# Optimization experiments

Hardware: AMD Instinct MI355X
Metric: run time of the kernel (lower is better)

## Reference

```python
import jax, jax.numpy as jnp
import numpy as np

B, L, D, H = 2, 4096, 128, 4


def setup_inputs() -> dict:
    key = jax.random.key(0)
    k_x, k_q, k_k, k_v, k_o = jax.random.split(key, 5)
    std = 0.02
    x = jax.random.normal(k_x, (B, L, D), dtype=jnp.float32)
    # torch nn.Linear(d_model, H*d_model).weight has shape [H*D, D]
    Wq = std * jax.random.normal(k_q, (H * D, D), dtype=jnp.float32)
    Wk = std * jax.random.normal(k_k, (H * D, D), dtype=jnp.float32)
    Wv = std * jax.random.normal(k_v, (H * D, D), dtype=jnp.float32)
    # W_O: Linear(H*d_model, d_model).weight -> [D, H*D]
    Wo = std * jax.random.normal(k_o, (D, H * D), dtype=jnp.float32)
    return {"x": x, "Wq": Wq, "Wk": Wk, "Wv": Wv, "Wo": Wo}


def reference(x, Wq, Wk, Wv, Wo):
    # project: weight rows indexed by (h, e); out = x @ W^T
    Wq3 = Wq.reshape(H, D, D)
    Wk3 = Wk.reshape(H, D, D)
    Wv3 = Wv.reshape(H, D, D)
    q = jnp.einsum('bld,hed->bhle', x, Wq3)  # [B,H,L,D]
    k = jnp.einsum('bld,hed->bhle', x, Wk3)
    v = jnp.einsum('bld,hed->bhle', x, Wv3)
    logits = jnp.einsum('bhle,bhme->bhlm', q, k)  # [B,H,L,L]
    causal_mask = jnp.triu(jnp.ones((L, L), dtype=bool), 1)
    neg = jnp.finfo(logits.dtype).min
    logits = jnp.where(causal_mask, neg, logits)
    attn = jax.nn.softmax(logits, axis=-1)
    ctx = jnp.einsum('bhlm,bhme->bhle', attn, v)  # [B,H,L,D]
    ctx = ctx.transpose(0, 2, 1, 3).reshape(B, L, H * D)
    y = ctx @ Wo.T  # [B,L,D]
    return y
```

## Files before the change

### kernel.cpp

```cpp
#include <hip/hip_runtime.h>

#define BB 2
#define LL 4096
#define DD 128
#define HH 4

typedef unsigned short u16;
typedef unsigned int u32;
typedef __attribute__((ext_vector_type(8))) short short8;
typedef __attribute__((ext_vector_type(4))) float floatx4;

union PFrag { short8 s; u32 u[4]; };

__device__ __forceinline__ u16 f2bf(float f) {
    union { float f; u32 u; } v; v.f = f;
    return (u16)((v.u + 0x7fffu + ((v.u >> 16) & 1u)) >> 16);
}

__device__ __forceinline__ void gld16(const u16* g, u16* l) {
    __builtin_amdgcn_global_load_lds((const __attribute__((address_space(1))) void*)g,
                                     (__attribute__((address_space(3))) void*)l, 16, 0, 0);
}

__device__ __forceinline__ int pfx(int t) {
    return (t < 16) ? (t - 8) : (t < 24) ? 8 + (t - 16) * 2 : 24 + (t - 24) * 3;
}

__global__ __launch_bounds__(256) void cvt_all(const float* __restrict__ x,
                                               const float* __restrict__ wq,
                                               const float* __restrict__ wk,
                                               const float* __restrict__ wv,
                                               const float* __restrict__ wo,
                                               u16* xb, u16* wqb, u16* wkb,
                                               u16* wvb, u16* wob,
                                               float* l_acc) {
    int z = blockIdx.y;
    if (z == 5) {
        int i = (blockIdx.x * 256 + threadIdx.x) * 4;
        if (i < 8 * LL) *(float4*)(l_acc + i) = (float4){0.f, 0.f, 0.f, 0.f};
        return;
    }
    const float* src; u16* dst; int n;
    if      (z == 0) { src = x;  dst = xb;  n = BB * LL * DD; }
    else if (z == 1) { src = wq; dst = wqb; n = HH * DD * DD; }
    else if (z == 2) { src = wk; dst = wkb; n = HH * DD * DD; }
    else if (z == 3) { src = wv; dst = wvb; n = HH * DD * DD; }
    else             { src = wo; dst = wob; n = DD * HH * DD; }
    int i = (blockIdx.x * 256 + threadIdx.x) * 4;
    if (i >= n) return;
    float4 v = *(const float4*)(src + i);
    ushort4 o;
    o.x = f2bf(v.x); o.y = f2bf(v.y); o.z = f2bf(v.z); o.w = f2bf(v.w);
    *(ushort4*)(dst + i) = o;
}

__global__ __launch_bounds__(256) void proj_qkv(const u16* __restrict__ xb,
                                                const u16* __restrict__ wqb,
                                                const u16* __restrict__ wkb,
                                                const u16* __restrict__ wvb,
                                                u16* __restrict__ Qb,
                                                u16* __restrict__ Kb,
                                                u16* __restrict__ Vt) {
    __shared__ __align__(16) u16 At[128 * 128];
    __shared__ __align__(16) u16 Wt[128 * 128];
    int lane = threadIdx.x & 63;
    int w    = threadIdx.x >> 6;
    int c = lane & 15, g = lane >> 4;
    int mt = blockIdx.x;
    int nt = blockIdx.y;
    int z = nt >> 2, h = nt & 3;
    const u16* Wg = ((z == 0) ? wqb : (z == 1) ? wkb : wvb) + h * 128 * DD;
    const u16* Ag = xb + (size_t)mt * 128 * DD;

#pragma unroll
    for (int i = 0; i < 8; i++) {
        int row = i * 16 + w * 4 + (lane >> 4);
        int cc  = (lane & 15) ^ (row & 15);
        gld16(Ag + row * DD + cc * 8, &At[(i * 16 + w * 4) * 128]);
    }
#pragma unroll
    for (int i = 0; i < 8; i++) {
        int row = i * 16 + w * 4 + (lane >> 4);
        int cc  = (lane & 15) ^ (row & 15);
        gld16(Wg + row * DD + cc * 8, &Wt[(i * 16 + w * 4) * 128]);
    }
    __syncthreads();

    const u16* Abuf = (z < 2) ? At : Wt;
    const u16* Bbuf = (z < 2) ? Wt : At;

    floatx4 acc[2][8];
#pragma unroll
    for (int m2 = 0; m2 < 2; m2++)
#pragma unroll
        for (int n2 = 0; n2 < 8; n2++) acc[m2][n2] = (floatx4){0.f, 0.f, 0.f, 0.f};

#pragma unroll
    for (int kk = 0; kk < 4; kk++) {
        short8 a0, a1, bf[8];
        {
            int r0 = w * 32 + c;
            int r1 = r0 + 16;
            a0 = *(const short8*)(&Abuf[r0 * 128 + (((g + 4 * kk) ^ (r0 & 15)) * 8)]);
            a1 = *(const short8*)(&Abuf[r1 * 128 + (((g + 4 * kk) ^ (r1 & 15)) * 8)]);
        }
#pragma unroll
        for (int n2 = 0; n2 < 8; n2++) {
            int rn = n2 * 16 + c;
            bf[n2] = *(const short8*)(&Bbuf[rn * 128 + (((g + 4 * kk) ^ (rn & 15)) * 8)]);
        }
#pragma unroll
        for (int n2 = 0; n2 < 8; n2++) {
            acc[0][n2] = __builtin_amdgcn_mfma_f32_16x16x32_bf16(a0, bf[n2], acc[0][n2], 0, 0, 0);
            acc[1][n2] = __builtin_amdgcn_mfma_f32_16x16x32_bf16(a1, bf[n2], acc[1][n2], 0, 0, 0);
        }
    }

    if (z < 2) {
        u16* out = (z == 0) ? Qb : Kb;
#pragma unroll
        for (int m2 = 0; m2 < 2; m2++)
#pragma unroll
            for (int r = 0; r < 4; r++) {
                int lg = mt * 128 + w * 32 + m2 * 16 + g * 4 + r;
                int b_ = lg >> 12, l = lg & 4095;
                u16* op = out + ((size_t)(b_ * HH + h) * LL + l) * DD + c;
#pragma unroll
                for (int n2 = 0; n2 < 8; n2++) op[n2 * 16] = f2bf(acc[m2][n2][r]);
            }
    } else {
        int b_ = mt >> 5;
        int lbase = (mt & 31) * 128;
#pragma unroll
        for (int m2 = 0; m2 < 2; m2++)
#pragma unroll
            for (int r = 0; r < 4; r++) {
                int e = w * 32 + m2 * 16 + g * 4 + r;
                u16* op = Vt + ((size_t)(b_ * HH + h) * DD + e) * LL + lbase + c;
#pragma unroll
                for (int n2 = 0; n2 < 8; n2++) op[n2 * 16] = f2bf(acc[m2][n2][r]);
            }
    }
}

__global__ __launch_bounds__(256) void flash_attn(const u16* __restrict__ Q,
                                                  const u16* __restrict__ K,
                                                  const u16* __restrict__ Vt,
                                                  float* __restrict__ ctx_base,
                                                  float* __restrict__ slots,
                                                  float* __restrict__ l_acc) {
    __shared__ __align__(16) u16 Kls[2][32 * 128];
    __shared__ __align__(16) u16 Vls[2][128 * 32];

    int lane = threadIdx.x & 63;
    int w    = threadIdx.x >> 6;
    int c = lane & 15, g = lane >> 4;

    int bid  = blockIdx.x;
    int head = bid & 7;
    int i    = bid >> 3;
    int t, ch;
    if      (i < 8)  { t = 8 + i; ch = 0; }
    else if (i < 24) { int f = i - 8;  t = 16 + (f >> 1); ch = f & 1; }
    else if (i < 48) { int f = i - 24; t = 24 + f / 3;    ch = f % 3; }
    else             { int d = i - 48; t = ((d & 3) << 3) + (7 - (d >> 2)); ch = d & 3; }

    int kstart = ch << 10;
    int kend   = min(t * 128 + 128, kstart + 1024);
    int nsteps = (kend - kstart) >> 5;

    int qb = t * 128 + w * 32;
    int my_steps = min(nsteps, ((qb + 31 - kstart) >> 5) + 1);

    short8 bq0[4], bq1[4];
    {
        const u16* qp0 = Q + ((size_t)head * LL + qb + c) * DD + g * 8;
        const u16* qp1 = qp0 + 16 * DD;
#pragma unroll
        for (int kk = 0; kk < 4; kk++) {
            bq0[kk] = *(const short8*)(qp0 + kk * 32);
            bq1[kk] = *(const short8*)(qp1 + kk * 32);
        }
    }

    floatx4 o0[8], o1[8];
#pragma unroll
    for (int tt = 0; tt < 8; tt++) {
        o0[tt] = (floatx4){0.f, 0.f, 0.f, 0.f};
        o1[tt] = (floatx4){0.f, 0.f, 0.f, 0.f};
    }
    float lsum0 = 0.f, lsum1 = 0.f;

    int s0 = c + (((g << 1) & 3) << 4);
    int s1 = c + ((((g << 1) | 1) & 3) << 4);
    bool hi = (g >= 2);

    const u16* Kg0 = K  + ((size_t)head * LL + kstart) * DD;
    const u16* Vg0 = Vt + (size_t)head * DD * LL + kstart;

    int q0 = w * 64 + lane;
    int r0 = q0 >> 4, cc0 = (q0 & 15) ^ (r0 & 15);
    int r1 = r0 + 16,  cc1 = (q0 & 15) ^ (r1 & 15);
    int e0 = q0 >> 2, c40 = (q0 & 3) * 8;
    int e1 = e0 + 64;

#define STAGE(s) {                                                          \
        int buf_ = (s) & 1; int kb_ = (s) << 5;                             \
        const u16* Kg = Kg0 + (size_t)kb_ * DD;                             \
        const u16* Vg = Vg0 + kb_;                                          \
        gld16(Kg + r0 * DD + cc0 * 8, &Kls[buf_][w * 512]);                 \
        gld16(Kg + r1 * DD + cc1 * 8, &Kls[buf_][2048 + w * 512]);          \
        gld16(Vg + (size_t)e0 * LL + c40, &Vls[buf_][w * 512]);             \
        gld16(Vg + (size_t)e1 * LL + c40, &Vls[buf_][2048 + w * 512]);      \
    }

    STAGE(0);

    for (int j = 0; j < nsteps; ++j) {
        __syncthreads();
        if (j + 1 < nsteps) STAGE(j + 1);
        if (j < my_steps) {
            int kb = kstart + (j << 5);
            const u16* Kb_ = &Kls[j & 1][0];
            const u16* Vb_ = &Vls[j & 1][0];

            floatx4 st00 = {0,0,0,0}, st01 = {0,0,0,0};
            floatx4 st10 = {0,0,0,0}, st11 = {0,0,0,0};
            {
                short8 ka[4];
#pragma unroll
                for (int kk = 0; kk < 4; kk++)
                    ka[kk] = *(const short8*)(Kb_ + c * 128 + (((g + 4 * kk) ^ c)) * 8);
#pragma unroll
                for (int kk = 0; kk < 4; kk++) {
                    st00 = __builtin_amdgcn_mfma_f32_16x16x32_bf16(ka[kk], bq0[kk], st00, 0, 0, 0);
                    st10 = __builtin_amdgcn_mfma_f32_16x16x32_bf16(ka[kk], bq1[kk], st10, 0, 0, 0);
                }
#pragma unroll
                for (int kk = 0; kk < 4; kk++)
                    ka[kk] = *(const short8*)(Kb_ + (16 + c) * 128 + (((g + 4 * kk) ^ c)) * 8);
#pragma unroll
                for (int kk = 0; kk < 4; kk++) {
                    st01 = __builtin_amdgcn_mfma_f32_16x16x32_bf16(ka[kk], bq0[kk], st01, 0, 0, 0);
                    st11 = __builtin_amdgcn_mfma_f32_16x16x32_bf16(ka[kk], bq1[kk], st11, 0, 0, 0);
                }
            }

            PFrag au0, au1;
#pragma unroll
            for (int qh = 0; qh < 2; qh++) {
                floatx4 sa = qh ? st10 : st00;
                floatx4 sb = qh ? st11 : st01;
                int qbh = qb + qh * 16;
                float p[8];
                if (kb + 31 > qbh) {
                    int q_c = qbh + c;
#pragma unroll
                    for (int r = 0; r < 4; r++) {
                        int k0 = kb + g * 4 + r;
                        p[r]     = (k0      <= q_c) ? sa[r] : -INFINITY;
                        p[4 + r] = (k0 + 16 <= q_c) ? sb[r] : -INFINITY;
                    }
                } else {
#pragma unroll
                    for (int r = 0; r < 4; r++) { p[r] = sa[r]; p[4 + r] = sb[r]; }
                }
                float ls = 0.f;
#pragma unroll
                for (int i2 = 0; i2 < 8; i2++) { p[i2] = __expf(p[i2]); ls += p[i2]; }
                if (qh) lsum1 += ls; else lsum0 += ls;

                u32 pk00 = (u32)f2bf(p[0]) | ((u32)f2bf(p[1]) << 16);
                u32 pk01 = (u32)f2bf(p[2]) | ((u32)f2bf(p[3]) << 16);
                u32 pk10 = (u32)f2bf(p[4]) | ((u32)f2bf(p[5]) << 16);
                u32 pk11 = (u32)f2bf(p[6]) | ((u32)f2bf(p[7]) << 16);
                u32 x00 = (u32)__shfl((int)pk00, s0), x10 = (u32)__shfl((int)pk10, s0);
                u32 x01 = (u32)__shfl((int)pk01, s0), x11 = (u32)__shfl((int)pk11, s0);
                u32 y00 = (u32)__shfl((int)pk00, s1), y10 = (u32)__shfl((int)pk10, s1);
                u32 y01 = (u32)__shfl((int)pk01, s1), y11 = (u32)__shfl((int)pk11, s1);
                PFrag* au = qh ? &au1 : &au0;
                au->u[0] = hi ? x10 : x00;
                au->u[1] = hi ? x11 : x01;
                au->u[2] = hi ? y10 : y00;
                au->u[3] = hi ? y11 : y01;
            }

#pragma unroll
            for (int tt = 0; tt < 8; tt++) {
                short8 vb = *(const short8*)(Vb_ + (tt * 16 + c) * 32 + g * 8);
                o0[tt] = __builtin_amdgcn_mfma_f32_16x16x32_bf16(au0.s, vb, o0[tt], 0, 0, 0);
                o1[tt] = __builtin_amdgcn_mfma_f32_16x16x32_bf16(au1.s, vb, o1[tt], 0, 0, 0);
            }
        }
    }
#undef STAGE

    lsum0 += __shfl_xor(lsum0, 16); lsum0 += __shfl_xor(lsum0, 32);
    lsum1 += __shfl_xor(lsum1, 16); lsum1 += __shfl_xor(lsum1, 32);
    if (g == 0) {
        atomicAdd(&l_acc[head * LL + qb + c],      lsum0);
        atomicAdd(&l_acc[head * LL + qb + 16 + c], lsum1);
    }

    bool diag = (ch == (t >> 3));
    float* dst0 = diag ? ctx_base + ((size_t)head * LL + t * 128) * 128
                       : slots + (size_t)(head * 48 + pfx(t) + ch) * 16384;
    dst0 += (size_t)(w * 32) * 128;
#pragma unroll
    for (int r = 0; r < 4; r++) {
        float* d0 = dst0 + (g * 4 + r) * 128 + c;
        float* d1 = d0 + 16 * 128;
#pragma unroll
        for (int tt = 0; tt < 8; tt++) {
            d0[tt * 16] = o0[tt][r];
            d1[tt * 16] = o1[tt][r];
        }
    }
}

__global__ __launch_bounds__(256) void norm_cast(const float* __restrict__ base,
                                                 const float* __restrict__ slots,
                                                 const float* __restrict__ l_acc,
                                                 u16* __restrict__ ctx) {
    int i = blockIdx.x * 256 + threadIdx.x;
    int e4 = i * 4;
    int col = e4 & 511;
    int bl  = e4 >> 9;
    int b_ = bl >> 12, l = bl & 4095;
    int h = col >> 7, d = col & 127;
    int head = b_ * HH + h;
    int t = l >> 7;
    int nx = t >> 3;

    float4 v = *(const float4*)(base + ((size_t)head * LL + l) * 128 + d);
    if (nx > 0) {
        int sb = head * 48 + pfx(t);
        for (int x = 0; x < nx; x++) {
            float4 sv = *(const float4*)(slots + (size_t)(sb + x) * 16384 + (l & 127) * 128 + d);
            v.x += sv.x; v.y += sv.y; v.z += sv.z; v.w += sv.w;
        }
    }
    float inv = 1.f / l_acc[head * LL + l];
    ushort4 o;
    o.x = f2bf(v.x * inv); o.y = f2bf(v.y * inv);
    o.z = f2bf(v.z * inv); o.w = f2bf(v.w * inv);
    *(ushort4*)(ctx + e4) = o;
}

__global__ __launch_bounds__(256) void proj_out(const u16* __restrict__ ctx,
                                                const u16* __restrict__ wo,
                                                float* __restrict__ y) {
    __shared__ __align__(16) u16 At[2][128 * 64];
    __shared__ __align__(16) u16 Wt[2][128 * 64];
    int lane = threadIdx.x & 63;
    int w    = threadIdx.x >> 6;
    int c = lane & 15, g = lane >> 4;
    int mt = blockIdx.x;
    const u16* Ag = ctx + (size_t)mt * 128 * 512;

#define PSTAGE(kc) {                                                        \
        int buf_ = (kc) & 1; int ks_ = (kc) * 64;                           \
        _Pragma("unroll")                                                   \
        for (int i = 0; i < 4; i++) {                                       \
            int row = i * 32 + w * 8 + (lane >> 3);                         \
            int cc  = (lane & 7) ^ (row & 7);                               \
            gld16(Ag + (size_t)row * 512 + ks_ + cc * 8,                    \
                  &At[buf_][(i * 32 + w * 8) * 64]);                        \
            gld16(wo + (size_t)row * 512 + ks_ + cc * 8,                    \
                  &Wt[buf_][(i * 32 + w * 8) * 64]);                        \
        }                                                                   \
    }

    floatx4 acc[2][8];
#pragma unroll
    for (int m2 = 0; m2 < 2; m2++)
#pragma unroll
        for (int n2 = 0; n2 < 8; n2++) acc[m2][n2] = (floatx4){0.f, 0.f, 0.f, 0.f};

    PSTAGE(0);
    for (int kc = 0; kc < 8; kc++) {
        __syncthreads();
        if (kc + 1 < 8) PSTAGE(kc + 1);
        int buf = kc & 1;
#pragma unroll
        for (int kk = 0; kk < 2; kk++) {
            int G = g + 4 * kk;
            short8 a0, a1, bf[8];
            {
                int ra = w * 32 + c;
                int rb = ra + 16;
                a0 = *(const short8*)(&At[buf][ra * 64 + ((G ^ (ra & 7)) * 8)]);
                a1 = *(const short8*)(&At[buf][rb * 64 + ((G ^ (rb & 7)) * 8)]);
            }
#pragma unroll
            for (int n2 = 0; n2 < 8; n2++) {
                int rn = n2 * 16 + c;
                bf[n2] = *(const short8*)(&Wt[buf][rn * 64 + ((G ^ (rn & 7)) * 8)]);
            }
#pragma unroll
            for (int n2 = 0; n2 < 8; n2++) {
                acc[0][n2] = __builtin_amdgcn_mfma_f32_16x16x32_bf16(a0, bf[n2], acc[0][n2], 0, 0, 0);
                acc[1][n2] = __builtin_amdgcn_mfma_f32_16x16x32_bf16(a1, bf[n2], acc[1][n2], 0, 0, 0);
            }
        }
    }
#undef PSTAGE

#pragma unroll
    for (int m2 = 0; m2 < 2; m2++)
#pragma unroll
        for (int r = 0; r < 4; r++) {
            int m = mt * 128 + w * 32 + m2 * 16 + g * 4 + r;
            float* yp = y + (size_t)m * 128 + c;
#pragma unroll
            for (int n2 = 0; n2 < 8; n2++) yp[n2 * 16] = acc[m2][n2][r];
        }
}

extern "C" void kernel_launch(void* const* d_in, const int* in_sizes, int n_in,
                              void* d_out, int out_size, void* d_ws, size_t ws_size,
                              hipStream_t stream) {
    const float* x  = (const float*)d_in[0];
    const float* Wq = (const float*)d_in[1];
    const float* Wk = (const float*)d_in[2];
    const float* Wv = (const float*)d_in[3];
    const float* Wo = (const float*)d_in[4];
    float* y = (float*)d_out;

    u16* ws  = (u16*)d_ws;
    u16* xb  = ws;
    u16* wqb = xb  + BB * LL * DD;
    u16* wkb = wqb + HH * DD * DD;
    u16* wvb = wkb + HH * DD * DD;
    u16* wob = wvb + HH * DD * DD;
    u16* Qb  = wob + DD * HH * DD;
    u16* Kb  = Qb  + BB * HH * LL * DD;
    u16* Vt  = Kb  + BB * HH * LL * DD;
    u16* ctx = Vt  + BB * HH * LL * DD;
    float* ctx_base = (float*)(ctx + (size_t)BB * LL * HH * DD);
    float* slots    = ctx_base + (size_t)8 * LL * 128;
    float* l_acc    = slots + (size_t)384 * 16384;

    cvt_all<<<dim3(1024, 6), 256, 0, stream>>>(x, Wq, Wk, Wv, Wo,
                                               xb, wqb, wkb, wvb, wob, l_acc);
    proj_qkv<<<dim3(64, 12), 256, 0, stream>>>(xb, wqb, wkb, wvb, Qb, Kb, Vt);
    flash_attn<<<dim3(640), 256, 0, stream>>>(Qb, Kb, Vt, ctx_base, slots, l_acc);
    norm_cast<<<dim3(4096), 256, 0, stream>>>(ctx_base, slots, l_acc, ctx);
    proj_out<<<dim3(64), 256, 0, stream>>>(ctx, wob, y);
}
```

Before: 171.1 us.

## Split attention keys into 512-wide chunks, store partials in bf16, load V directly

The causal attention work is re-split into key chunks of 512 instead of 1024, raising the block count from 640 to 1152 for better load balance across CUs. Partial context outputs and slots are now stored as bf16 instead of fp32, halving the write and read traffic between flash_attn and norm_cast. V tiles are read straight from global memory into registers instead of being staged through LDS, and packing of P to bf16 uses the packed conversion intrinsic. In exchange, norm_cast must sum more partial slots, and accumulating bf16 partials loses some precision.

Result: slower. 178.2 us (+4.2%).

```diff
diff --git a/kernel.cpp b/kernel.cpp
--- a/kernel.cpp
+++ b/kernel.cpp
@@ -1,4 +1,5 @@
 #include <hip/hip_runtime.h>
+#include <hip/hip_bf16.h>
 
 #define BB 2
 #define LL 4096
@@ -17,13 +18,25 @@
     return (u16)((v.u + 0x7fffu + ((v.u >> 16) & 1u)) >> 16);
 }
 
+__device__ __forceinline__ float bf2f(u16 u) {
+    union { u32 u; float f; } v; v.u = (u32)u << 16;
+    return v.f;
+}
+
+__device__ __forceinline__ u32 pk2bf(float a, float b) {
+    union { __hip_bfloat162 h; u32 u; } v;
+    v.h = __float22bfloat162_rn(float2{a, b});
+    return v.u;
+}
+
 __device__ __forceinline__ void gld16(const u16* g, u16* l) {
     __builtin_amdgcn_global_load_lds((const __attribute__((address_space(1))) void*)g,
                                      (__attribute__((address_space(3))) void*)l, 16, 0, 0);
 }
 
-__device__ __forceinline__ int pfx(int t) {
-    return (t < 16) ? (t - 8) : (t < 24) ? 8 + (t - 16) * 2 : 24 + (t - 24) * 3;
+__device__ __forceinline__ int pfx2(int t) {
+    int a = t >> 2, b = t & 3;
+    return 2 * a * (a - 1) + a * b;
 }
 
 __global__ __launch_bounds__(256) void cvt_all(const float* __restrict__ x,
@@ -146,11 +159,10 @@
 __global__ __launch_bounds__(256) void flash_attn(const u16* __restrict__ Q,
                                                   const u16* __restrict__ K,
                                                   const u16* __restrict__ Vt,
-                                                  float* __restrict__ ctx_base,
-                                                  float* __restrict__ slots,
+                                                  u16* __restrict__ basep,
+                                                  u16* __restrict__ slots,
                                                   float* __restrict__ l_acc) {
     __shared__ __align__(16) u16 Kls[2][32 * 128];
-    __shared__ __align__(16) u16 Vls[2][128 * 32];
 
     int lane = threadIdx.x & 63;
     int w    = threadIdx.x >> 6;
@@ -160,13 +172,19 @@
     int head = bid & 7;
     int i    = bid >> 3;
     int t, ch;
-    if      (i < 8)  { t = 8 + i; ch = 0; }
-    else if (i < 24) { int f = i - 8;  t = 16 + (f >> 1); ch = f & 1; }
-    else if (i < 48) { int f = i - 24; t = 24 + f / 3;    ch = f % 3; }
-    else             { int d = i - 48; t = ((d & 3) << 3) + (7 - (d >> 2)); ch = d & 3; }
-
-    int kstart = ch << 10;
-    int kend   = min(t * 128 + 128, kstart + 1024);
+    if (i < 120) {
+        int rem = i; ch = 0;
+        while (rem >= 29 - 4 * ch) { rem -= 29 - 4 * ch; ch++; }
+        t = 31 - rem;
+    } else {
+        int j = i - 120;
+        if (j < 8)       { t = 30 - 4 * j;        ch = (t - 2) >> 2; }
+        else if (j < 16) { t = 29 - 4 * (j - 8);  ch = (t - 1) >> 2; }
+        else             { t = 28 - 4 * (j - 16); ch = t >> 2; }
+    }
+
+    int kstart = ch << 9;
+    int kend   = min((t + 1) << 7, kstart + 512);
     int nsteps = (kend - kstart) >> 5;
 
     int qb = t * 128 + w * 32;
@@ -196,22 +214,17 @@
     bool hi = (g >= 2);
 
     const u16* Kg0 = K  + ((size_t)head * LL + kstart) * DD;
-    const u16* Vg0 = Vt + (size_t)head * DD * LL + kstart;
+    const u16* vp0 = Vt + ((size_t)head * DD + c) * LL + kstart + g * 8;
 
     int q0 = w * 64 + lane;
     int r0 = q0 >> 4, cc0 = (q0 & 15) ^ (r0 & 15);
     int r1 = r0 + 16,  cc1 = (q0 & 15) ^ (r1 & 15);
-    int e0 = q0 >> 2, c40 = (q0 & 3) * 8;
-    int e1 = e0 + 64;
 
 #define STAGE(s) {                                                          \
         int buf_ = (s) & 1; int kb_ = (s) << 5;                             \
         const u16* Kg = Kg0 + (size_t)kb_ * DD;                             \
-        const u16* Vg = Vg0 + kb_;                                          \
         gld16(Kg + r0 * DD + cc0 * 8, &Kls[buf_][w * 512]);                 \
         gld16(Kg + r1 * DD + cc1 * 8, &Kls[buf_][2048 + w * 512]);          \
-        gld16(Vg + (size_t)e0 * LL + c40, &Vls[buf_][w * 512]);             \
-        gld16(Vg + (size_t)e1 * LL + c40, &Vls[buf_][2048 + w * 512]);      \
     }
 
     STAGE(0);
@@ -222,7 +235,11 @@
         if (j < my_steps) {
             int kb = kstart + (j << 5);
             const u16* Kb_ = &Kls[j & 1][0];
-            const u16* Vb_ = &Vls[j & 1][0];
+
+            short8 vb[8];
+#pragma unroll
+            for (int tt = 0; tt < 8; tt++)
+                vb[tt] = *(const short8*)(vp0 + (size_t)tt * 16 * LL + (j << 5));
 
             floatx4 st00 = {0,0,0,0}, st01 = {0,0,0,0};
             floatx4 st10 = {0,0,0,0}, st11 = {0,0,0,0};
@@ -270,10 +287,10 @@
                 for (int i2 = 0; i2 < 8; i2++) { p[i2] = __expf(p[i2]); ls += p[i2]; }
                 if (qh) lsum1 += ls; else lsum0 += ls;
 
-                u32 pk00 = (u32)f2bf(p[0]) | ((u32)f2bf(p[1]) << 16);
-                u32 pk01 = (u32)f2bf(p[2]) | ((u32)f2bf(p[3]) << 16);
-                u32 pk10 = (u32)f2bf(p[4]) | ((u32)f2bf(p[5]) << 16);
-                u32 pk11 = (u32)f2bf(p[6]) | ((u32)f2bf(p[7]) << 16);
+                u32 pk00 = pk2bf(p[0], p[1]);
+                u32 pk01 = pk2bf(p[2], p[3]);
+                u32 pk10 = pk2bf(p[4], p[5]);
+                u32 pk11 = pk2bf(p[6], p[7]);
                 u32 x00 = (u32)__shfl((int)pk00, s0), x10 = (u32)__shfl((int)pk10, s0);
                 u32 x01 = (u32)__shfl((int)pk01, s0), x11 = (u32)__shfl((int)pk11, s0);
                 u32 y00 = (u32)__shfl((int)pk00, s1), y10 = (u32)__shfl((int)pk10, s1);
@@ -287,9 +304,8 @@
 
 #pragma unroll
             for (int tt = 0; tt < 8; tt++) {
-                short8 vb = *(const short8*)(Vb_ + (tt * 16 + c) * 32 + g * 8);
-                o0[tt] = __builtin_amdgcn_mfma_f32_16x16x32_bf16(au0.s, vb, o0[tt], 0, 0, 0);
-                o1[tt] = __builtin_amdgcn_mfma_f32_16x16x32_bf16(au1.s, vb, o1[tt], 0, 0, 0);
+                o0[tt] = __builtin_amdgcn_mfma_f32_16x16x32_bf16(au0.s, vb[tt], o0[tt], 0, 0, 0);
+                o1[tt] = __builtin_amdgcn_mfma_f32_16x16x32_bf16(au1.s, vb[tt], o1[tt], 0, 0, 0);
             }
         }
     }
@@ -302,24 +318,24 @@
         atomicAdd(&l_acc[head * LL + qb + 16 + c], lsum1);
     }
 
-    bool diag = (ch == (t >> 3));
-    float* dst0 = diag ? ctx_base + ((size_t)head * LL + t * 128) * 128
-                       : slots + (size_t)(head * 48 + pfx(t) + ch) * 16384;
+    bool diag = (kstart + 512 >= ((t + 1) << 7));
+    u16* dst0 = diag ? basep + ((size_t)head * LL + t * 128) * 128
+                     : slots + ((size_t)(head * 112 + pfx2(t) + ch)) * 16384;
     dst0 += (size_t)(w * 32) * 128;
 #pragma unroll
     for (int r = 0; r < 4; r++) {
-        float* d0 = dst0 + (g * 4 + r) * 128 + c;
-        float* d1 = d0 + 16 * 128;
+        u16* d0 = dst0 + (g * 4 + r) * 128 + c;
+        u16* d1 = d0 + 16 * 128;
 #pragma unroll
         for (int tt = 0; tt < 8; tt++) {
-            d0[tt * 16] = o0[tt][r];
-            d1[tt * 16] = o1[tt][r];
-        }
-    }
-}
-
-__global__ __launch_bounds__(256) void norm_cast(const float* __restrict__ base,
-                                                 const float* __restrict__ slots,
+            d0[tt * 16] = f2bf(o0[tt][r]);
+            d1[tt * 16] = f2bf(o1[tt][r]);
+        }
+    }
+}
+
+__global__ __launch_bounds__(256) void norm_cast(const u16* __restrict__ basep,
+                                                 const u16* __restrict__ slots,
                                                  const float* __restrict__ l_acc,
                                                  u16* __restrict__ ctx) {
     int i = blockIdx.x * 256 + threadIdx.x;
@@ -330,20 +346,21 @@
     int h = col >> 7, d = col & 127;
     int head = b_ * HH + h;
     int t = l >> 7;
-    int nx = t >> 3;
-
-    float4 v = *(const float4*)(base + ((size_t)head * LL + l) * 128 + d);
+    int nx = t >> 2;
+
+    ushort4 bv = *(const ushort4*)(basep + ((size_t)head * LL + l) * 128 + d);
+    float v0 = bf2f(bv.x), v1 = bf2f(bv.y), v2 = bf2f(bv.z), v3 = bf2f(bv.w);
     if (nx > 0) {
-        int sb = head * 48 + pfx(t);
+        int sb = head * 112 + pfx2(t);
         for (int x = 0; x < nx; x++) {
-            float4 sv = *(const float4*)(slots + (size_t)(sb + x) * 16384 + (l & 127) * 128 + d);
-            v.x += sv.x; v.y += sv.y; v.z += sv.z; v.w += sv.w;
+            ushort4 sv = *(const ushort4*)(slots + (size_t)(sb + x) * 16384 + (l & 127) * 128 + d);
+            v0 += bf2f(sv.x); v1 += bf2f(sv.y); v2 += bf2f(sv.z); v3 += bf2f(sv.w);
         }
     }
     float inv = 1.f / l_acc[head * LL + l];
     ushort4 o;
-    o.x = f2bf(v.x * inv); o.y = f2bf(v.y * inv);
-    o.z = f2bf(v.z * inv); o.w = f2bf(v.w * inv);
+    o.x = f2bf(v0 * inv); o.y = f2bf(v1 * inv);
+    o.z = f2bf(v2 * inv); o.w = f2bf(v3 * inv);
     *(ushort4*)(ctx + e4) = o;
 }
 
@@ -437,14 +454,14 @@
     u16* Kb  = Qb  + BB * HH * LL * DD;
     u16* Vt  = Kb  + BB * HH * LL * DD;
     u16* ctx = Vt  + BB * HH * LL * DD;
-    float* ctx_base = (float*)(ctx + (size_t)BB * LL * HH * DD);
-    float* slots    = ctx_base + (size_t)8 * LL * 128;
-    float* l_acc    = slots + (size_t)384 * 16384;
+    u16* basep = ctx + (size_t)BB * LL * HH * DD;
+    u16* slots = basep + (size_t)8 * LL * 128;
+    float* l_acc = (float*)(slots + (size_t)896 * 16384);
 
     cvt_all<<<dim3(1024, 6), 256, 0, stream>>>(x, Wq, Wk, Wv, Wo,
                                                xb, wqb, wkb, wvb, wob, l_acc);
     proj_qkv<<<dim3(64, 12), 256, 0, stream>>>(xb, wqb, wkb, wvb, Qb, Kb, Vt);
-    flash_attn<<<dim3(640), 256, 0, stream>>>(Qb, Kb, Vt, ctx_base, slots, l_acc);
-    norm_cast<<<dim3(4096), 256, 0, stream>>>(ctx_base, slots, l_acc, ctx);
+    flash_attn<<<dim3(1152), 256, 0, stream>>>(Qb, Kb, Vt, basep, slots, l_acc);
+    norm_cast<<<dim3(4096), 256, 0, stream>>>(basep, slots, l_acc, ctx);
     proj_out<<<dim3(64), 256, 0, stream>>>(ctx, wob, y);
 }
```
